# Kernel optimization log

Hardware: AMD Instinct MI355X
Metric: run time of the kernel (lower is better)

Reference implementation:

```python
import jax, jax.numpy as jnp
import numpy as np

GAMMA = 0.99
LMBDA = 0.95
B, T = 8192, 2048


def setup_inputs() -> dict:
    key = jax.random.key(0)
    k1, k2, k3, k4 = jax.random.split(key, 4)
    reward = jax.random.normal(k1, (B, T), dtype=jnp.float32)
    terminated = jax.random.randint(k2, (B, T), 0, 2, dtype=jnp.int32)
    value = jax.random.normal(k3, (B, T), dtype=jnp.float32)
    next_value = jax.random.normal(k4, (B, T), dtype=jnp.float32)
    return {"reward": reward, "terminated": terminated, "value": value, "next_value": next_value}


def reference(reward, terminated, value, next_value):
    # not_done: [B, T]
    not_done = 1.0 - terminated.astype(jnp.float32)
    # delta_t = r_t + gamma * V(s_{t+1}) * nd_t - V(s_t)   (all elementwise, [B, T])
    delta = reward + GAMMA * next_value * not_done - value
    gl = GAMMA * LMBDA

    # backward recurrence over time: gae_t = delta_t + gamma*lmbda*nd_t*gae_{t+1}
    def step(gae, xs):  # gae: [B]
        d_t, nd_t = xs  # each [B]
        gae = d_t + gl * nd_t * gae
        return gae, gae

    xs = (jnp.swapaxes(delta, 0, 1), jnp.swapaxes(not_done, 0, 1))  # [T, B]
    init = jnp.zeros((reward.shape[0],), dtype=reward.dtype)
    _, adv_tb = jax.lax.scan(step, init, xs, reverse=True)  # [T, B], time-ordered
    advantages = jnp.swapaxes(adv_tb, 0, 1)  # [B, T]
    returns = advantages + value
    return advantages, returns
```

## Files before the change

kernel.cpp:

```cpp
#include <hip/hip_runtime.h>


constexpr float GAMMA_F = 0.99f;
constexpr float GL      = 0.99f * 0.95f;
constexpr int   T_LEN   = 2048;
constexpr int   PER_LANE = 8;
constexpr int   SEG     = 64 * PER_LANE;
constexpr int   NBLK    = T_LEN / SEG;
constexpr int   WPB     = 4;

typedef float  vf4 __attribute__((ext_vector_type(4)));

constexpr float gl_pow8() {
    double p = 1.0;
    for (int i = 0; i < 8; ++i) p *= (double)GL;
    return (float)p;
}
constexpr float GL8 = gl_pow8();

struct Raw {
    float4 r0, r1, v0, v1, n0, n1;
    int4   t0, t1;
};

__device__ inline Raw load_blk(const float* __restrict__ r, const int* __restrict__ t,
                               const float* __restrict__ v, const float* __restrict__ n,
                               long base) {
    Raw x;
    const float4* r4 = reinterpret_cast<const float4*>(r + base);
    const int4*   t4 = reinterpret_cast<const int4*>(t + base);
    const float4* v4 = reinterpret_cast<const float4*>(v + base);
    const float4* n4 = reinterpret_cast<const float4*>(n + base);
    x.r0 = r4[0]; x.r1 = r4[1];
    x.t0 = t4[0]; x.t1 = t4[1];
    x.v0 = v4[0]; x.v1 = v4[1];
    x.n0 = n4[0]; x.n1 = n4[1];
    return x;
}

__device__ inline void st_nt4(float* p, float a, float b, float c, float d) {
    vf4 val = {a, b, c, d};
    __builtin_nontemporal_store(val, reinterpret_cast<vf4*>(p));
}

__global__ __launch_bounds__(256)
void gae_kernel(const float* __restrict__ reward,
                const int*   __restrict__ term,
                const float* __restrict__ value,
                const float* __restrict__ next_value,
                float* __restrict__ adv_out,
                float* __restrict__ ret_out,
                int rows) {
    const int wid  = threadIdx.x >> 6;
    const int lane = threadIdx.x & 63;
    const int row  = blockIdx.x * WPB + wid;
    if (row >= rows) return;

    const long rowbase = (long)row * T_LEN;

    Raw cur = load_blk(reward, term, value, next_value,
                       rowbase + (long)(NBLK - 1) * SEG + lane * PER_LANE);
    float g_carry = 0.0f;

#pragma unroll
    for (int c = NBLK - 1; c >= 0; --c) {
        Raw nxt;
        if (c > 0)
            nxt = load_blk(reward, term, value, next_value,
                           rowbase + (long)(c - 1) * SEG + lane * PER_LANE);

        float rr[8] = {cur.r0.x, cur.r0.y, cur.r0.z, cur.r0.w,
                       cur.r1.x, cur.r1.y, cur.r1.z, cur.r1.w};
        int   tt[8] = {cur.t0.x, cur.t0.y, cur.t0.z, cur.t0.w,
                       cur.t1.x, cur.t1.y, cur.t1.z, cur.t1.w};
        float vv[8] = {cur.v0.x, cur.v0.y, cur.v0.z, cur.v0.w,
                       cur.v1.x, cur.v1.y, cur.v1.z, cur.v1.w};
        float nn[8] = {cur.n0.x, cur.n0.y, cur.n0.z, cur.n0.w,
                       cur.n1.x, cur.n1.y, cur.n1.z, cur.n1.w};
        float d[8];
        unsigned mask = 0;
#pragma unroll
        for (int j = 0; j < 8; ++j) {
            const float nd = (float)(1 - tt[j]);
            d[j]  = fmaf(GAMMA_F * nd, nn[j], rr[j]) - vv[j];
            mask |= (tt[j] ? 0u : 1u) << j;
        }

        float Bc = 0.0f;
#pragma unroll
        for (int j = PER_LANE - 1; j >= 0; --j) {
            const float a = ((mask >> j) & 1u) ? GL : 0.0f;
            Bc = fmaf(a, Bc, d[j]);
        }
        float A = (mask == 0xFFu) ? GL8 : 0.0f;

#pragma unroll
        for (int off = 1; off < 64; off <<= 1) {
            const float A2 = __shfl_down(A, off, 64);
            const float B2 = __shfl_down(Bc, off, 64);
            if (lane + off < 64) {
                Bc = fmaf(A, B2, Bc);
                A *= A2;
            }
        }

        const float As1 = __shfl_down(A, 1, 64);
        const float Bs1 = __shfl_down(Bc, 1, 64);
        const float gin = (lane == 63) ? g_carry : fmaf(As1, g_carry, Bs1);

        const float A0 = __shfl(A, 0, 64);
        const float B0 = __shfl(Bc, 0, 64);

        float g = gin;
        float ga[8], ro[8];
#pragma unroll
        for (int j = PER_LANE - 1; j >= 0; --j) {
            const float a = ((mask >> j) & 1u) ? GL : 0.0f;
            g = fmaf(a, g, d[j]);
            ga[j] = g;
            ro[j] = g + vv[j];
        }
        const long ob = rowbase + (long)c * SEG + lane * PER_LANE;
        st_nt4(adv_out + ob,     ga[0], ga[1], ga[2], ga[3]);
        st_nt4(adv_out + ob + 4, ga[4], ga[5], ga[6], ga[7]);
        st_nt4(ret_out + ob,     ro[0], ro[1], ro[2], ro[3]);
        st_nt4(ret_out + ob + 4, ro[4], ro[5], ro[6], ro[7]);

        g_carry = fmaf(A0, g_carry, B0);
        if (c > 0) cur = nxt;
    }
}

extern "C" void kernel_launch(void* const* d_in, const int* in_sizes, int n_in,
                              void* d_out, int out_size, void* d_ws, size_t ws_size,
                              hipStream_t stream) {
    const float* reward     = (const float*)d_in[0];
    const int*   terminated = (const int*)d_in[1];
    const float* value      = (const float*)d_in[2];
    const float* next_value = (const float*)d_in[3];

    const int total = in_sizes[0];
    const int rows  = total / T_LEN;

    float* adv = (float*)d_out;
    float* ret = adv + (long)total;

    const int block = 64 * WPB;
    const int grid  = (rows + WPB - 1) / WPB;
    gae_kernel<<<grid, block, 0, stream>>>(reward, terminated, value, next_value,
                                           adv, ret, rows);
}
```

Baseline: 343.5 us.

## Load whole row upfront and scan all segments concurrently per wave

New measurement: 334.7 us. 2.5% less time.

```diff
diff --git a/kernel.cpp b/kernel.cpp
--- a/kernel.cpp
+++ b/kernel.cpp
@@ -9,7 +9,7 @@
 constexpr int   NBLK    = T_LEN / SEG;
 constexpr int   WPB     = 4;
 
-typedef float  vf4 __attribute__((ext_vector_type(4)));
+typedef float vf4 __attribute__((ext_vector_type(4)));
 
 constexpr float gl_pow8() {
     double p = 1.0;
@@ -17,26 +17,6 @@
     return (float)p;
 }
 constexpr float GL8 = gl_pow8();
-
-struct Raw {
-    float4 r0, r1, v0, v1, n0, n1;
-    int4   t0, t1;
-};
-
-__device__ inline Raw load_blk(const float* __restrict__ r, const int* __restrict__ t,
-                               const float* __restrict__ v, const float* __restrict__ n,
-                               long base) {
-    Raw x;
-    const float4* r4 = reinterpret_cast<const float4*>(r + base);
-    const int4*   t4 = reinterpret_cast<const int4*>(t + base);
-    const float4* v4 = reinterpret_cast<const float4*>(v + base);
-    const float4* n4 = reinterpret_cast<const float4*>(n + base);
-    x.r0 = r4[0]; x.r1 = r4[1];
-    x.t0 = t4[0]; x.t1 = t4[1];
-    x.v0 = v4[0]; x.v1 = v4[1];
-    x.n0 = n4[0]; x.n1 = n4[1];
-    return x;
-}
 
 __device__ inline void st_nt4(float* p, float a, float b, float c, float d) {
     vf4 val = {a, b, c, d};
@@ -58,76 +38,97 @@
 
     const long rowbase = (long)row * T_LEN;
 
-    Raw cur = load_blk(reward, term, value, next_value,
-                       rowbase + (long)(NBLK - 1) * SEG + lane * PER_LANE);
-    float g_carry = 0.0f;
+    float4 rr4[NBLK][2], vv4[NBLK][2], nn4[NBLK][2];
+    int4   tt4[NBLK][2];
+#pragma unroll
+    for (int b = 0; b < NBLK; ++b) {
+        const long base = rowbase + (long)b * SEG + lane * PER_LANE;
+        const float4* r4 = reinterpret_cast<const float4*>(reward + base);
+        const int4*   t4 = reinterpret_cast<const int4*>(term + base);
+        const float4* v4 = reinterpret_cast<const float4*>(value + base);
+        const float4* n4 = reinterpret_cast<const float4*>(next_value + base);
+        rr4[b][0] = r4[0]; rr4[b][1] = r4[1];
+        tt4[b][0] = t4[0]; tt4[b][1] = t4[1];
+        vv4[b][0] = v4[0]; vv4[b][1] = v4[1];
+        nn4[b][0] = n4[0]; nn4[b][1] = n4[1];
+    }
 
+    float    d[NBLK][PER_LANE], vv[NBLK][PER_LANE];
+    unsigned mask[NBLK];
+    float    A[NBLK], Bc[NBLK];
 #pragma unroll
-    for (int c = NBLK - 1; c >= 0; --c) {
-        Raw nxt;
-        if (c > 0)
-            nxt = load_blk(reward, term, value, next_value,
-                           rowbase + (long)(c - 1) * SEG + lane * PER_LANE);
-
-        float rr[8] = {cur.r0.x, cur.r0.y, cur.r0.z, cur.r0.w,
-                       cur.r1.x, cur.r1.y, cur.r1.z, cur.r1.w};
-        int   tt[8] = {cur.t0.x, cur.t0.y, cur.t0.z, cur.t0.w,
-                       cur.t1.x, cur.t1.y, cur.t1.z, cur.t1.w};
-        float vv[8] = {cur.v0.x, cur.v0.y, cur.v0.z, cur.v0.w,
-                       cur.v1.x, cur.v1.y, cur.v1.z, cur.v1.w};
-        float nn[8] = {cur.n0.x, cur.n0.y, cur.n0.z, cur.n0.w,
-                       cur.n1.x, cur.n1.y, cur.n1.z, cur.n1.w};
-        float d[8];
-        unsigned mask = 0;
+    for (int b = 0; b < NBLK; ++b) {
+        const float rr[8] = {rr4[b][0].x, rr4[b][0].y, rr4[b][0].z, rr4[b][0].w,
+                             rr4[b][1].x, rr4[b][1].y, rr4[b][1].z, rr4[b][1].w};
+        const int   tt[8] = {tt4[b][0].x, tt4[b][0].y, tt4[b][0].z, tt4[b][0].w,
+                             tt4[b][1].x, tt4[b][1].y, tt4[b][1].z, tt4[b][1].w};
+        const float vvl[8] = {vv4[b][0].x, vv4[b][0].y, vv4[b][0].z, vv4[b][0].w,
+                              vv4[b][1].x, vv4[b][1].y, vv4[b][1].z, vv4[b][1].w};
+        const float nn[8] = {nn4[b][0].x, nn4[b][0].y, nn4[b][0].z, nn4[b][0].w,
+                             nn4[b][1].x, nn4[b][1].y, nn4[b][1].z, nn4[b][1].w};
+        unsigned m = 0;
 #pragma unroll
         for (int j = 0; j < 8; ++j) {
             const float nd = (float)(1 - tt[j]);
-            d[j]  = fmaf(GAMMA_F * nd, nn[j], rr[j]) - vv[j];
-            mask |= (tt[j] ? 0u : 1u) << j;
+            d[b][j]  = fmaf(GAMMA_F * nd, nn[j], rr[j]) - vvl[j];
+            vv[b][j] = vvl[j];
+            m |= (tt[j] ? 0u : 1u) << j;
         }
-
-        float Bc = 0.0f;
+        mask[b] = m;
+        float bc = 0.0f;
 #pragma unroll
         for (int j = PER_LANE - 1; j >= 0; --j) {
-            const float a = ((mask >> j) & 1u) ? GL : 0.0f;
-            Bc = fmaf(a, Bc, d[j]);
+            const float a = ((m >> j) & 1u) ? GL : 0.0f;
+            bc = fmaf(a, bc, d[b][j]);
         }
-        float A = (mask == 0xFFu) ? GL8 : 0.0f;
+        Bc[b] = bc;
+        A[b]  = (m == 0xFFu) ? GL8 : 0.0f;
+    }
 
 #pragma unroll
-        for (int off = 1; off < 64; off <<= 1) {
-            const float A2 = __shfl_down(A, off, 64);
-            const float B2 = __shfl_down(Bc, off, 64);
+    for (int off = 1; off < 64; off <<= 1) {
+#pragma unroll
+        for (int b = 0; b < NBLK; ++b) {
+            const float A2 = __shfl_down(A[b], off, 64);
+            const float B2 = __shfl_down(Bc[b], off, 64);
             if (lane + off < 64) {
-                Bc = fmaf(A, B2, Bc);
-                A *= A2;
+                Bc[b] = fmaf(A[b], B2, Bc[b]);
+                A[b] *= A2;
             }
         }
+    }
 
-        const float As1 = __shfl_down(A, 1, 64);
-        const float Bs1 = __shfl_down(Bc, 1, 64);
-        const float gin = (lane == 63) ? g_carry : fmaf(As1, g_carry, Bs1);
+    float As1[NBLK], Bs1[NBLK], A0[NBLK], B0[NBLK];
+#pragma unroll
+    for (int b = 0; b < NBLK; ++b) {
+        As1[b] = __shfl_down(A[b], 1, 64);
+        Bs1[b] = __shfl_down(Bc[b], 1, 64);
+        A0[b]  = __shfl(A[b], 0, 64);
+        B0[b]  = __shfl(Bc[b], 0, 64);
+    }
 
-        const float A0 = __shfl(A, 0, 64);
-        const float B0 = __shfl(Bc, 0, 64);
+    float carry[NBLK];
+    carry[NBLK - 1] = 0.0f;
+#pragma unroll
+    for (int b = NBLK - 2; b >= 0; --b)
+        carry[b] = fmaf(A0[b + 1], carry[b + 1], B0[b + 1]);
 
-        float g = gin;
+#pragma unroll
+    for (int b = 0; b < NBLK; ++b) {
+        float g = (lane == 63) ? carry[b] : fmaf(As1[b], carry[b], Bs1[b]);
         float ga[8], ro[8];
 #pragma unroll
         for (int j = PER_LANE - 1; j >= 0; --j) {
-            const float a = ((mask >> j) & 1u) ? GL : 0.0f;
-            g = fmaf(a, g, d[j]);
+            const float a = ((mask[b] >> j) & 1u) ? GL : 0.0f;
+            g = fmaf(a, g, d[b][j]);
             ga[j] = g;
-            ro[j] = g + vv[j];
+            ro[j] = g + vv[b][j];
         }
-        const long ob = rowbase + (long)c * SEG + lane * PER_LANE;
+        const long ob = rowbase + (long)b * SEG + lane * PER_LANE;
         st_nt4(adv_out + ob,     ga[0], ga[1], ga[2], ga[3]);
         st_nt4(adv_out + ob + 4, ga[4], ga[5], ga[6], ga[7]);
         st_nt4(ret_out + ob,     ro[0], ro[1], ro[2], ro[3]);
         st_nt4(ret_out + ob + 4, ro[4], ro[5], ro[6], ro[7]);
-
-        g_carry = fmaf(A0, g_carry, B0);
-        if (c > 0) cur = nxt;
     }
 }
 
```
